# Kernel tuning notes

Hardware: AMD Instinct MI355X
Metric: run time of the kernel (lower is better)

## Reference

```python
import jax, jax.numpy as jnp
import numpy as np

N_NODES = 200000
N_EDGES = 800000
N_GRAPHS = 2048
N_SUB = 32768
E_SUB = 131072
F_IN = 38
H0, H1, H2 = 256, 128, 64
BN_EPS = 1e-5


def _l2norm(x):
    n = jnp.sqrt(jnp.sum(x * x, axis=1, keepdims=True))
    return x / jnp.maximum(n, 1e-12)


def _bn(x):
    # fresh nn.BatchNorm1d in training mode: gamma=1, beta=0, biased var
    m = x.mean(0, keepdims=True)
    v = x.var(0, keepdims=True)
    return (x - m) * jax.lax.rsqrt(v + BN_EPS)


def _seg_bn(x, seg, num_seg):
    # per-subgraph BatchNorm (source loops over subgraphs, BN stats per subgraph)
    ones = jnp.ones((x.shape[0],), x.dtype)
    cnt = jnp.maximum(jax.ops.segment_sum(ones, seg, num_seg), 1.0)[:, None]
    m = jax.ops.segment_sum(x, seg, num_seg) / cnt
    v = jax.ops.segment_sum(x * x, seg, num_seg) / cnt - m * m
    return (x - m[seg]) * jax.lax.rsqrt(jnp.maximum(v[seg], 0.0) + BN_EPS)


def _seg_mean(x, seg, num_seg):
    ones = jnp.ones((x.shape[0],), x.dtype)
    cnt = jnp.maximum(jax.ops.segment_sum(ones, seg, num_seg), 1.0)[:, None]
    return jax.ops.segment_sum(x, seg, num_seg) / cnt


def _gcn(x, W, b, src, dst):
    N = x.shape[0]
    h = x @ W
    deg = jnp.ones((N,), x.dtype).at[dst].add(1.0)  # in-degree + self loop
    dinv = jax.lax.rsqrt(deg)
    coef = (dinv[src] * dinv[dst])[:, None]
    agg = jnp.zeros_like(h).at[dst].add(coef * h[src]) + (dinv * dinv)[:, None] * h
    return agg + b


def setup_inputs() -> dict:
    key = jax.random.key(0)
    ks = jax.random.split(key, 40)

    def lin(k, fi, fo):
        return jax.random.normal(k, (fi, fo), jnp.float32) / np.float32(np.sqrt(fi))

    inp = {}
    inp['x'] = jax.random.normal(ks[0], (N_NODES, F_IN), jnp.float32)
    inp['edge_index'] = jax.random.randint(ks[1], (2, N_EDGES), 0, N_NODES)
    inp['batch'] = jnp.sort(jax.random.randint(ks[2], (N_NODES,), 0, N_GRAPHS))
    inp['target_x'] = jax.random.normal(ks[3], (N_GRAPHS, F_IN), jnp.float32)
    inp['pos_x'] = jax.random.normal(ks[4], (N_SUB, F_IN), jnp.float32)
    inp['pos_edge_index'] = jax.random.randint(ks[5], (2, E_SUB), 0, N_SUB)
    inp['pos_batch'] = jnp.sort(jax.random.randint(ks[6], (N_SUB,), 0, N_GRAPHS))
    inp['neg_x'] = jax.random.normal(ks[7], (N_SUB, F_IN), jnp.float32)
    inp['neg_edge_index'] = jax.random.randint(ks[8], (2, E_SUB), 0, N_SUB)
    inp['neg_batch'] = jnp.sort(jax.random.randint(ks[9], (N_SUB,), 0, N_GRAPHS))

    # main GCN encoder
    inp['enc_W0'] = lin(ks[10], F_IN, H0); inp['enc_b0'] = jnp.zeros((H0,), jnp.float32)
    inp['enc_W1'] = lin(ks[11], H0, H1);  inp['enc_b1'] = jnp.zeros((H1,), jnp.float32)
    inp['enc_W2'] = lin(ks[12], H1, H2);  inp['enc_b2'] = jnp.zeros((H2,), jnp.float32)
    # decoder (bias=False)
    inp['dec_W0'] = lin(ks[13], H2, H1)
    inp['dec_W1'] = lin(ks[14], H1, H0)
    inp['dec_W2'] = lin(ks[15], H0, F_IN)
    # node MLP encoder
    inp['node_W0'] = lin(ks[16], F_IN, H0); inp['node_b0'] = jnp.zeros((H0,), jnp.float32)
    inp['node_W1'] = lin(ks[17], H0, H1);  inp['node_b1'] = jnp.zeros((H1,), jnp.float32)
    inp['node_W2'] = lin(ks[18], H1, H2);  inp['node_b2'] = jnp.zeros((H2,), jnp.float32)
    # subgraph GCN encoder (last layer of encode_subgraph reuses self.encoders[-1])
    inp['sub_W0'] = lin(ks[19], F_IN, H0); inp['sub_b0'] = jnp.zeros((H0,), jnp.float32)
    inp['sub_W1'] = lin(ks[20], H0, H1);  inp['sub_b1'] = jnp.zeros((H1,), jnp.float32)
    # classifier
    inp['cls_W0'] = lin(ks[21], H2, H1);  inp['cls_b0'] = jnp.zeros((H1,), jnp.float32)
    inp['cls_W1'] = lin(ks[22], H1, 16);  inp['cls_b1'] = jnp.zeros((16,), jnp.float32)
    inp['cls_W2'] = lin(ks[23], 16, 1);   inp['cls_b2'] = jnp.zeros((1,), jnp.float32)
    return inp


def reference(x, edge_index, batch, target_x, pos_x, pos_edge_index, pos_batch,
              neg_x, neg_edge_index, neg_batch,
              enc_W0, enc_b0, enc_W1, enc_b1, enc_W2, enc_b2,
              dec_W0, dec_W1, dec_W2,
              node_W0, node_b0, node_W1, node_b1, node_W2, node_b2,
              sub_W0, sub_b0, sub_W1, sub_b1,
              cls_W0, cls_b0, cls_W1, cls_b1, cls_W2, cls_b2):
    relu = jax.nn.relu
    src, dst = edge_index[0], edge_index[1]

    # encode: GCN -> ReLU -> BN (x2), GCN, L2 normalize
    h = _bn(relu(_gcn(x, enc_W0, enc_b0, src, dst)))
    h = _bn(relu(_gcn(h, enc_W1, enc_b1, src, dst)))
    z = _l2norm(_gcn(h, enc_W2, enc_b2, src, dst))

    # decode: Linear(no bias) ReLU stack, sigmoid output
    r = relu(z @ dec_W0)
    r = relu(r @ dec_W1)
    x_recon = jax.nn.sigmoid(r @ dec_W2)

    z_pool = _seg_mean(z, batch, N_GRAPHS)

    # encode_node on target node features
    t = _bn(relu(target_x @ node_W0 + node_b0))
    t = _bn(relu(t @ node_W1 + node_b1))
    target_z = _l2norm(t @ node_W2 + node_b2)

    # batched subgraph encoding: GCN stack with per-subgraph BatchNorm;
    # last layer reuses main encoders[-1] weights (as in source encode_subgraph)
    def encode_sub(sx, sei, seg):
        s, d = sei[0], sei[1]
        sh = _seg_bn(relu(_gcn(sx, sub_W0, sub_b0, s, d)), seg, N_GRAPHS)
        sh = _seg_bn(relu(_gcn(sh, sub_W1, sub_b1, s, d)), seg, N_GRAPHS)
        return _l2norm(_gcn(sh, enc_W2, enc_b2, s, d))

    pos_z = encode_sub(pos_x, pos_edge_index, pos_batch)
    pos_pool = _seg_mean(pos_z, pos_batch, N_GRAPHS)
    neg_z = encode_sub(neg_x, neg_edge_index, neg_batch)
    neg_pool = _seg_mean(neg_z, neg_batch, N_GRAPHS)

    # classify negative subgraph pools
    p = relu(neg_pool @ cls_W0 + cls_b0)
    p = relu(p @ cls_W1 + cls_b1)
    neg_pred = jax.nn.sigmoid(p @ cls_W2 + cls_b2)

    return (x_recon, z_pool, target_z, pos_pool, neg_pool, neg_pred)
```

## Files before the change

### kernel.cpp

```cpp
#include <hip/hip_runtime.h>
#include <hip/hip_bf16.h>
#include <math.h>

#define N_NODES  200000
#define N_EDGES  800000
#define N_GRAPHS 2048
#define N_SUB    32768
#define E_SUB    131072
#define F_IN     38
#define H0       256
#define H1       128
#define H2       64
#define BN_EPS   1e-5f

typedef __hip_bfloat16 bf16;
typedef __attribute__((ext_vector_type(8))) short short8;
typedef __attribute__((ext_vector_type(4))) short short4v;
typedef __attribute__((ext_vector_type(4))) float float4v;

static __host__ __device__ inline int cdiv(int a, int b) { return (a + b - 1) / b; }

__device__ inline float ldf(const float* p, size_t i) { return p[i]; }
__device__ inline float ldf(const bf16* p, size_t i)  { return __bfloat162float(p[i]); }
__device__ inline void  stf(float* p, size_t i, float v) { p[i] = v; }
__device__ inline void  stf(bf16* p, size_t i, float v)  { p[i] = __float2bfloat16(v); }

__device__ inline float2 ldf2(const float* p, size_t i) { return ((const float2*)p)[i]; }
__device__ inline float2 ldf2(const bf16* p, size_t i) {
    __hip_bfloat162 v = ((const __hip_bfloat162*)p)[i];
    return make_float2(__bfloat162float(v.x), __bfloat162float(v.y));
}
__device__ inline void stf2(float* p, size_t i, float2 v) { ((float2*)p)[i] = v; }
__device__ inline void stf2(bf16* p, size_t i, float2 v) {
    __hip_bfloat162 t;
    t.x = __float2bfloat16(v.x);
    t.y = __float2bfloat16(v.y);
    ((__hip_bfloat162*)p)[i] = t;
}

__device__ inline short bf16bits(float v) {
    bf16 t = __float2bfloat16(v);
    return *reinterpret_cast<short*>(&t);
}
__device__ inline float bits2f(short s) {
    return __bfloat162float(*reinterpret_cast<const bf16*>(&s));
}

__global__ void k_zero(float* __restrict__ p, int n) {
    int i = blockIdx.x * 256 + threadIdx.x;
    if (i < n) p[i] = 0.f;
}

__global__ void k_count(const int* __restrict__ dst, int* __restrict__ cnt, int e) {
    int i = blockIdx.x * 256 + threadIdx.x;
    if (i < e) atomicAdd(&cnt[dst[i]], 1);
}

__global__ void k_dinv(const int* __restrict__ cnt, float* __restrict__ dinv, int n) {
    int i = blockIdx.x * 256 + threadIdx.x;
    if (i < n) dinv[i] = rsqrtf(1.0f + (float)cnt[i]);
}

__global__ void k_scan_sum(const int* __restrict__ cnt, int* __restrict__ bsum, int n) {
    __shared__ int tmp[256];
    int t = threadIdx.x;
    int i = blockIdx.x * 256 + t;
    tmp[t] = (i < n) ? cnt[i] : 0;
    __syncthreads();
    for (int off = 128; off > 0; off >>= 1) {
        if (t < off) tmp[t] += tmp[t + off];
        __syncthreads();
    }
    if (t == 0) bsum[blockIdx.x] = tmp[0];
}

__global__ void k_scan_top(int* __restrict__ bsum, int nb) {
    __shared__ int tmp[1024];
    int t = threadIdx.x;
    int v = (t < nb) ? bsum[t] : 0;
    tmp[t] = v;
    __syncthreads();
    for (int off = 1; off < 1024; off <<= 1) {
        int a = (t >= off) ? tmp[t - off] : 0;
        __syncthreads();
        tmp[t] += a;
        __syncthreads();
    }
    if (t < nb) bsum[t] = tmp[t] - v;
}

__global__ void k_scan_apply(const int* __restrict__ cnt, const int* __restrict__ bsum,
                             int* __restrict__ rowptr, int n) {
    __shared__ int tmp[256];
    int t = threadIdx.x;
    int i = blockIdx.x * 256 + t;
    int v = (i < n) ? cnt[i] : 0;
    tmp[t] = v;
    __syncthreads();
    for (int off = 1; off < 256; off <<= 1) {
        int a = (t >= off) ? tmp[t - off] : 0;
        __syncthreads();
        tmp[t] += a;
        __syncthreads();
    }
    int excl = tmp[t] - v + bsum[blockIdx.x];
    if (i < n) rowptr[i] = excl;
    if (i == n - 1) rowptr[n] = excl + v;
}

__global__ void k_fill(const int* __restrict__ src, const int* __restrict__ dst,
                       const int* __restrict__ rowptr, int* __restrict__ cursor,
                       int* __restrict__ col, int e) {
    int i = blockIdx.x * 256 + threadIdx.x;
    if (i < e) {
        int d = dst[i];
        int p = rowptr[d] + atomicAdd(&cursor[d], 1);
        col[p] = src[i];
    }
}

__global__ void k_gbound(const int* __restrict__ seg, int n, int nseg,
                         int* __restrict__ gstart) {
    int i = blockIdx.x * 256 + threadIdx.x;
    if (i >= n) return;
    int s = seg[i];
    if (i == 0) {
        for (int g = 0; g <= s; ++g) gstart[g] = 0;
    } else {
        int p = seg[i - 1];
        for (int g = p + 1; g <= s; ++g) gstart[g] = i;
    }
    if (i == n - 1) {
        for (int g = s + 1; g <= nseg; ++g) gstart[g] = n;
    }
}

__global__ void k_merge(const float* __restrict__ px, const float* __restrict__ nx,
                        const int* __restrict__ pei, const int* __restrict__ nei,
                        const int* __restrict__ pb, const int* __restrict__ nbt,
                        float* __restrict__ mx, int* __restrict__ msrc,
                        int* __restrict__ mdst, int* __restrict__ mb) {
    int stride = gridDim.x * 256;
    for (int i = blockIdx.x * 256 + threadIdx.x; i < N_SUB * F_IN; i += stride) {
        mx[i] = px[i];
        mx[(size_t)N_SUB * F_IN + i] = nx[i];
    }
    for (int i = blockIdx.x * 256 + threadIdx.x; i < E_SUB; i += stride) {
        msrc[i] = pei[i];
        mdst[i] = pei[E_SUB + i];
        msrc[E_SUB + i] = nei[i] + N_SUB;
        mdst[E_SUB + i] = nei[E_SUB + i] + N_SUB;
    }
    for (int i = blockIdx.x * 256 + threadIdx.x; i < N_SUB; i += stride) {
        mb[i] = pb[i];
        mb[N_SUB + i] = nbt[i] + N_GRAPHS;
    }
}

template <typename TI, typename TO, int PPN>
__global__ __launch_bounds__(256) void k_gather5(
    const TI* __restrict__ h, const float* __restrict__ dinv,
    const int* __restrict__ rowptr, const int* __restrict__ col,
    TO* __restrict__ o, int n, int M2, int S2,
    const float* __restrict__ bias, int relu)
{
    const int NPW = 64 / PPN;
    int g0 = threadIdx.x / PPN;
    int pr = threadIdx.x % PPN;
    int nA = (blockIdx.x * 4 + threadIdx.y) * (2 * NPW) + g0 * 2;
    if (nA >= n) return;
    int nB = nA + 1;
    bool okB = nB < n;
    bool pld = pr < M2, pst = pr < S2;

    int2 rp = *(const int2*)(rowptr + nA);
    float diA = dinv[nA];
    float diB = okB ? dinv[nB] : 0.f;
    float2 vsA = make_float2(0.f, 0.f), vsB = make_float2(0.f, 0.f);
    if (pld) {
        vsA = ldf2(h, (size_t)nA * M2 + pr);
        if (okB) vsB = ldf2(h, (size_t)nB * M2 + pr);
    }
    int peB = okB ? rowptr[nA + 2] : rp.y;

    int pA = rp.x, peA = rp.y;
    int pB = peA;

    int sA1 = 0, sB1 = 0;
    float dA0 = 0.f, dB0 = 0.f;
    float2 vA0 = make_float2(0.f, 0.f), vB0 = make_float2(0.f, 0.f);

    if (pA < peA) {
        int s0 = col[pA];
        sA1 = (pA + 1 < peA) ? col[pA + 1] : 0;
        dA0 = dinv[s0];
        if (pld) vA0 = ldf2(h, (size_t)s0 * M2 + pr);
    }
    if (pB < peB) {
        int s0 = col[pB];
        sB1 = (pB + 1 < peB) ? col[pB + 1] : 0;
        dB0 = dinv[s0];
        if (pld) vB0 = ldf2(h, (size_t)s0 * M2 + pr);
    }

    float2 accA, accB;
    accA.x = diA * diA * vsA.x; accA.y = diA * diA * vsA.y;
    accB.x = diB * diB * vsB.x; accB.y = diB * diB * vsB.y;

    while (pA < peA && pB < peB) {
        int sA2 = (pA + 2 < peA) ? col[pA + 2] : 0;
        int sB2 = (pB + 2 < peB) ? col[pB + 2] : 0;
        float2 vA1 = (pA + 1 < peA && pld) ? ldf2(h, (size_t)sA1 * M2 + pr)
                                           : make_float2(0.f, 0.f);
        float2 vB1 = (pB + 1 < peB && pld) ? ldf2(h, (size_t)sB1 * M2 + pr)
                                           : make_float2(0.f, 0.f);
        float dA1 = (pA + 1 < peA) ? dinv[sA1] : 0.f;
        float dB1 = (pB + 1 < peB) ? dinv[sB1] : 0.f;
        float cfA = dA0 * diA, cfB = dB0 * diB;
        accA.x += cfA * vA0.x; accA.y += cfA * vA0.y;
        accB.x += cfB * vB0.x; accB.y += cfB * vB0.y;
        sA1 = sA2; vA0 = vA1; dA0 = dA1;
        sB1 = sB2; vB0 = vB1; dB0 = dB1;
        ++pA; ++pB;
    }
    while (pA < peA) {
        int sA2 = (pA + 2 < peA) ? col[pA + 2] : 0;
        float2 vA1 = (pA + 1 < peA && pld) ? ldf2(h, (size_t)sA1 * M2 + pr)
                                           : make_float2(0.f, 0.f);
        float dA1 = (pA + 1 < peA) ? dinv[sA1] : 0.f;
        float cfA = dA0 * diA;
        accA.x += cfA * vA0.x; accA.y += cfA * vA0.y;
        sA1 = sA2; vA0 = vA1; dA0 = dA1; ++pA;
    }
    while (pB < peB) {
        int sB2 = (pB + 2 < peB) ? col[pB + 2] : 0;
        float2 vB1 = (pB + 1 < peB && pld) ? ldf2(h, (size_t)sB1 * M2 + pr)
                                           : make_float2(0.f, 0.f);
        float dB1 = (pB + 1 < peB) ? dinv[sB1] : 0.f;
        float cfB = dB0 * diB;
        accB.x += cfB * vB0.x; accB.y += cfB * vB0.y;
        sB1 = sB2; vB0 = vB1; dB0 = dB1; ++pB;
    }

    if (pst) {
        float2 rA = accA;
        if (bias && pld) { rA.x += bias[2 * pr]; rA.y += bias[2 * pr + 1]; }
        if (relu) { rA.x = fmaxf(rA.x, 0.f); rA.y = fmaxf(rA.y, 0.f); }
        stf2(o, (size_t)nA * S2 + pr, rA);
        if (okB) {
            float2 rB = accB;
            if (bias && pld) { rB.x += bias[2 * pr]; rB.y += bias[2 * pr + 1]; }
            if (relu) { rB.x = fmaxf(rB.x, 0.f); rB.y = fmaxf(rB.y, 0.f); }
            stf2(o, (size_t)nB * S2 + pr, rB);
        }
    }
}

template <typename TI, typename TO>
static void launch_gather(const TI* h, const float* dinv, const int* rowptr,
                          const int* col, TO* o, int n, int M, int Sout,
                          const float* bias, int relu, hipStream_t stream) {
    dim3 b(64, 4);
    int M2 = M >> 1, S2 = Sout >> 1;
    if (S2 > 32)
        k_gather5<TI, TO, 64><<<cdiv(n, 8), b, 0, stream>>>(h, dinv, rowptr, col, o,
                                                            n, M2, S2, bias, relu);
    else
        k_gather5<TI, TO, 32><<<cdiv(n, 16), b, 0, stream>>>(h, dinv, rowptr, col, o,
                                                             n, M2, S2, bias, relu);
}

template <typename TO, int LPR>
__global__ __launch_bounds__(256) void k_gather6(
    const bf16* __restrict__ h, const float* __restrict__ dinv,
    const int* __restrict__ rowptr, const int* __restrict__ col,
    TO* __restrict__ o, int n, const float* __restrict__ bias, int relu)
{
    const int W = LPR * 8;
    const int NG = 64 / LPR;
    const int g = threadIdx.x / LPR;
    const int c0 = (threadIdx.x % LPR) * 8;
    const int nA = (blockIdx.x * 4 + threadIdx.y) * (2 * NG) + g * 2;
    const int nB = nA + 1;
    if (nA >= n) return;
    const bool okB = nB < n;

    int2 rp = *(const int2*)(rowptr + nA);
    int peB = okB ? rowptr[nB + 1] : rp.y;
    float diA = dinv[nA];
    float diB = okB ? dinv[nB] : 0.f;
    short8 zed = {0, 0, 0, 0, 0, 0, 0, 0};
    short8 slA = *(const short8*)(h + (size_t)nA * W + c0);
    short8 slB = okB ? *(const short8*)(h + (size_t)nB * W + c0) : zed;

    int pA = rp.x, peA = rp.y;
    int pB = rp.y;

    float accA[8], accB[8];
    float qA = diA * diA, qB = diB * diB;
#pragma unroll
    for (int j = 0; j < 8; ++j) {
        accA[j] = qA * bits2f(slA[j]);
        accB[j] = qB * bits2f(slB[j]);
    }

    int sA1 = 0, sB1 = 0;
    float dA0 = 0.f, dB0 = 0.f;
    short8 vA0 = zed, vB0 = zed;
    if (pA < peA) {
        int s0 = col[pA];
        sA1 = (pA + 1 < peA) ? col[pA + 1] : 0;
        dA0 = dinv[s0];
        vA0 = *(const short8*)(h + (size_t)s0 * W + c0);
    }
    if (pB < peB) {
        int s0 = col[pB];
        sB1 = (pB + 1 < peB) ? col[pB + 1] : 0;
        dB0 = dinv[s0];
        vB0 = *(const short8*)(h + (size_t)s0 * W + c0);
    }

    while (__any(pA < peA || pB < peB)) {
        if (pA < peA) {
            int sA2 = (pA + 2 < peA) ? col[pA + 2] : 0;
            short8 vA1 = zed;
            float dA1 = 0.f;
            if (pA + 1 < peA) {
                vA1 = *(const short8*)(h + (size_t)sA1 * W + c0);
                dA1 = dinv[sA1];
            }
            float cf = dA0 * diA;
#pragma unroll
            for (int j = 0; j < 8; ++j) accA[j] += cf * bits2f(vA0[j]);
            vA0 = vA1; dA0 = dA1; sA1 = sA2; ++pA;
        }
        if (pB < peB) {
            int sB2 = (pB + 2 < peB) ? col[pB + 2] : 0;
            short8 vB1 = zed;
            float dB1 = 0.f;
            if (pB + 1 < peB) {
                vB1 = *(const short8*)(h + (size_t)sB1 * W + c0);
                dB1 = dinv[sB1];
            }
            float cf = dB0 * diB;
#pragma unroll
            for (int j = 0; j < 8; ++j) accB[j] += cf * bits2f(vB0[j]);
            vB0 = vB1; dB0 = dB1; sB1 = sB2; ++pB;
        }
    }

    float bv[8];
#pragma unroll
    for (int j = 0; j < 8; ++j) bv[j] = 0.f;
    if (bias) {
        float4 b0 = *(const float4*)(bias + c0);
        float4 b1 = *(const float4*)(bias + c0 + 4);
        bv[0] = b0.x; bv[1] = b0.y; bv[2] = b0.z; bv[3] = b0.w;
        bv[4] = b1.x; bv[5] = b1.y; bv[6] = b1.z; bv[7] = b1.w;
    }

    auto store_row = [&](int node, float* acc) {
        float r[8];
#pragma unroll
        for (int j = 0; j < 8; ++j) {
            r[j] = acc[j] + bv[j];
            if (relu) r[j] = fmaxf(r[j], 0.f);
        }
        size_t off = (size_t)node * W + c0;
        if constexpr (sizeof(TO) == 2) {
            short8 pk;
#pragma unroll
            for (int j = 0; j < 8; ++j) pk[j] = bf16bits(r[j]);
            *(short8*)((bf16*)o + off) = pk;
        } else {
            float4 f0 = {r[0], r[1], r[2], r[3]};
            float4 f1 = {r[4], r[5], r[6], r[7]};
            *(float4*)((float*)o + off) = f0;
            *(float4*)((float*)o + off + 4) = f1;
        }
    };
    store_row(nA, accA);
    if (okB) store_row(nB, accB);
}

template <typename TO>
static void launch_gather6(const bf16* h, const float* dinv, const int* rowptr,
                           const int* col, TO* o, int n, int W,
                           const float* bias, int relu, hipStream_t stream) {
    dim3 b(64, 4);
    if (W == 128)
        k_gather6<TO, 16><<<cdiv(n, 32), b, 0, stream>>>(h, dinv, rowptr, col, o, n,
                                                         bias, relu);
    else
        k_gather6<TO, 8><<<cdiv(n, 64), b, 0, stream>>>(h, dinv, rowptr, col, o, n,
                                                        bias, relu);
}

template <int K, int M, int Mp>
__device__ inline void wpack1(const float* __restrict__ W, bf16* __restrict__ o, int j) {
    int kk = j & 31;
    int rem = j >> 5;
    int ncol = rem % Mp;
    int s = rem / Mp;
    int k = s * 32 + kk;
    float v = (k < K && ncol < M) ? W[(size_t)k * M + ncol] : 0.f;
    o[j] = __float2bfloat16(v);
}

__global__ void k_wpack_all(const float* __restrict__ eW0, const float* __restrict__ eW1,
                            const float* __restrict__ eW2, const float* __restrict__ dW0,
                            const float* __restrict__ dW1, const float* __restrict__ dW2,
                            const float* __restrict__ sW0, const float* __restrict__ sW1,
                            bf16* __restrict__ arena) {
    for (int i = blockIdx.x * 256 + threadIdx.x; i < 159744; i += gridDim.x * 256) {
        if (i < 16384)       wpack1<38, 256, 256>(eW0, arena, i);
        else if (i < 49152)  wpack1<256, 128, 128>(eW1, arena + 16384, i - 16384);
        else if (i < 57344)  wpack1<128, 64, 64>(eW2, arena + 49152, i - 49152);
        else if (i < 65536)  wpack1<64, 128, 128>(dW0, arena + 57344, i - 57344);
        else if (i < 98304)  wpack1<128, 256, 256>(dW1, arena + 65536, i - 65536);
        else if (i < 110592) wpack1<256, 38, 48>(dW2, arena + 98304, i - 98304);
        else if (i < 126976) wpack1<38, 256, 256>(sW0, arena + 110592, i - 110592);
        else                 wpack1<256, 128, 128>(sW1, arena + 126976, i - 126976);
    }
}

template <int K, int M, int Mp>
__global__ void k_wfold(const float* __restrict__ W, const float* __restrict__ mu,
                        const float* __restrict__ sc, bf16* __restrict__ Wb,
                        float* __restrict__ bout) {
    const int tot = (K / 32) * Mp * 32;
    for (int i = blockIdx.x * 256 + threadIdx.x; i < tot; i += gridDim.x * 256) {
        int kk = i & 31;
        int rem = i >> 5;
        int ncol = rem % Mp;
        int s = rem / Mp;
        int k = s * 32 + kk;
        float v = (k < K && ncol < M) ? sc[k] * W[(size_t)k * M + ncol] : 0.f;
        Wb[i] = __float2bfloat16(v);
    }
    if (blockIdx.x == 0 && threadIdx.x < M) {
        int j = threadIdx.x;
        float s = 0.f;
        for (int k = 0; k < K; ++k) s -= mu[k] * sc[k] * W[(size_t)k * M + j];
        bout[j] = s;
    }
}

template <typename TC, int NT, int S, int BNM>
__global__ __launch_bounds__(256, 3) void k_mfma_gemm(
    const bf16* __restrict__ A, const bf16* __restrict__ Wb,
    TC* __restrict__ C, int M, int MC,
    const float* __restrict__ bias, int act,
    const float* __restrict__ mu, const float* __restrict__ sc,
    const int* __restrict__ seg)
{
    const int SA = S * 32;
    const int Mp = NT * 16;
    const int lane = threadIdx.x;
    const int wave = threadIdx.y;
    const int row0 = blockIdx.x * 64 + wave * 16;
    const int qr = lane >> 4;
    const int lc = lane & 15;

    short8 af[S];
    {
        const bf16* arow = A + (size_t)(row0 + lc) * SA + qr * 8;
#pragma unroll
        for (int s = 0; s < S; ++s) af[s] = *(const short8*)(arow + s * 32);
    }
    if (BNM == 2) {
        size_t bnbase = (size_t)seg[row0 + lc] * SA;
#pragma unroll
        for (int s = 0; s < S; ++s) {
            int kb = s * 32 + qr * 8;
            const float* mp = mu + bnbase + kb;
            const float* sp = sc + bnbase + kb;
            float4 m0 = *(const float4*)mp, m1 = *(const float4*)(mp + 4);
            float4 s0 = *(const float4*)sp, s1 = *(const float4*)(sp + 4);
            float av[8];
#pragma unroll
            for (int j = 0; j < 8; ++j) av[j] = bits2f(af[s][j]);
            av[0] = (av[0] - m0.x) * s0.x; av[1] = (av[1] - m0.y) * s0.y;
            av[2] = (av[2] - m0.z) * s0.z; av[3] = (av[3] - m0.w) * s0.w;
            av[4] = (av[4] - m1.x) * s1.x; av[5] = (av[5] - m1.y) * s1.y;
            av[6] = (av[6] - m1.z) * s1.z; av[7] = (av[7] - m1.w) * s1.w;
#pragma unroll
            for (int j = 0; j < 8; ++j) af[s][j] = bf16bits(av[j]);
        }
    }

    float4v acc[NT];
#pragma unroll
    for (int t = 0; t < NT; ++t) acc[t] = (float4v){0.f, 0.f, 0.f, 0.f};

    const bf16* wrow = Wb + (size_t)lc * 32 + qr * 8;
#pragma unroll
    for (int s = 0; s < S; ++s) {
        short8 wfv[NT];
#pragma unroll
        for (int t = 0; t < NT; ++t)
            wfv[t] = *(const short8*)(wrow + ((size_t)s * Mp + t * 16) * 32);
#pragma unroll
        for (int t = 0; t < NT; ++t)
            acc[t] = __builtin_amdgcn_mfma_f32_16x16x32_bf16(wfv[t], af[s], acc[t], 0, 0, 0);
    }

    const int row = row0 + lc;
#pragma unroll
    for (int t = 0; t < NT; ++t) {
        int c0 = t * 16 + qr * 4;
        if (c0 >= M) continue;
        float v[4];
#pragma unroll
        for (int r = 0; r < 4; ++r) v[r] = acc[t][r];
        if (bias) {
            if (c0 + 3 < M) {
                float4 bv = *(const float4*)(bias + c0);
                v[0] += bv.x; v[1] += bv.y; v[2] += bv.z; v[3] += bv.w;
            } else {
#pragma unroll
                for (int r = 0; r < 4; ++r) if (c0 + r < M) v[r] += bias[c0 + r];
            }
        }
#pragma unroll
        for (int r = 0; r < 4; ++r) {
            if (act == 1) v[r] = fmaxf(v[r], 0.f);
            else if (act == 2) v[r] = 1.f / (1.f + expf(-v[r]));
        }
        if (c0 + 3 < M) {
            if constexpr (sizeof(TC) == 2) {
                short4v pk = {bf16bits(v[0]), bf16bits(v[1]), bf16bits(v[2]), bf16bits(v[3])};
                *(short4v*)((bf16*)C + (size_t)row * MC + c0) = pk;
            } else {
                stf2((float*)C, ((size_t)row * MC + c0) >> 1, make_float2(v[0], v[1]));
                stf2((float*)C, ((size_t)row * MC + c0 + 2) >> 1, make_float2(v[2], v[3]));
            }
        } else {
#pragma unroll
            for (int r = 0; r < 4; ++r)
                if (c0 + r < M) stf(C, (size_t)row * MC + c0 + r, v[r]);
        }
    }
}

template <typename TC, int BNM>
static void launch_mfma(const bf16* A, const bf16* Wb, TC* C, int n, int SA,
                        int Mp, int M, int MC, const float* bias, int act,
                        const float* mu, const float* sc, const int* seg,
                        hipStream_t stream) {
    dim3 b(64, 4);
    int g = n / 64;
    if (SA == 64 && Mp == 256)
        k_mfma_gemm<TC, 16, 2, BNM><<<g, b, 0, stream>>>(A, Wb, C, M, MC, bias, act, mu, sc, seg);
    else if (SA == 256 && Mp == 128)
        k_mfma_gemm<TC, 8, 8, BNM><<<g, b, 0, stream>>>(A, Wb, C, M, MC, bias, act, mu, sc, seg);
    else if (SA == 128 && Mp == 64)
        k_mfma_gemm<TC, 4, 4, BNM><<<g, b, 0, stream>>>(A, Wb, C, M, MC, bias, act, mu, sc, seg);
}

__global__ __launch_bounds__(256) void k_l0stats(
    const bf16* __restrict__ Y0, const bf16* __restrict__ W0b,
    const float* __restrict__ b0, float* __restrict__ sum,
    float* __restrict__ sumsq, int ntiles)
{
    __shared__ float ls[4][512];
    const int lane = threadIdx.x;
    const int wave = threadIdx.y;
    const int lc = lane & 15, qr = lane >> 4;

    float bv[16];
#pragma unroll
    for (int t = 0; t < 16; ++t) bv[t] = b0[t * 16 + lc];

    float sReg[16], qReg[16];
#pragma unroll
    for (int t = 0; t < 16; ++t) { sReg[t] = 0.f; qReg[t] = 0.f; }

    for (int tile = blockIdx.x; tile < ntiles; tile += gridDim.x) {
        const int row0 = tile * 64 + wave * 16;
        const bf16* arow = Y0 + (size_t)(row0 + lc) * 64 + qr * 8;
        float4v acc[16];
#pragma unroll
        for (int t = 0; t < 16; ++t) acc[t] = (float4v){0.f, 0.f, 0.f, 0.f};
#pragma unroll
        for (int s = 0; s < 2; ++s) {
            short8 af = *(const short8*)(arow + s * 32);
#pragma unroll
            for (int t = 0; t < 16; ++t) {
                short8 wf = *(const short8*)(W0b + ((size_t)(s * 256 + t * 16 + lc)) * 32 + qr * 8);
                acc[t] = __builtin_amdgcn_mfma_f32_16x16x32_bf16(af, wf, acc[t], 0, 0, 0);
            }
        }
#pragma unroll
        for (int t = 0; t < 16; ++t) {
            float s4 = 0.f, q4 = 0.f;
#pragma unroll
            for (int r = 0; r < 4; ++r) {
                float v = fmaxf(acc[t][r] + bv[t], 0.f);
                v = bits2f(bf16bits(v));
                s4 += v;
                q4 += v * v;
            }
            s4 += __shfl_xor(s4, 16, 64); s4 += __shfl_xor(s4, 32, 64);
            q4 += __shfl_xor(q4, 16, 64); q4 += __shfl_xor(q4, 32, 64);
            sReg[t] += s4;
            qReg[t] += q4;
        }
    }
    if (lane < 16) {
#pragma unroll
        for (int t = 0; t < 16; ++t) {
            ls[wave][t * 16 + lc] = sReg[t];
            ls[wave][256 + t * 16 + lc] = qReg[t];
        }
    }
    __syncthreads();
    int tid = wave * 64 + lane;
    if (tid < 256) {
        atomicAdd(&sum[tid], ls[0][tid] + ls[1][tid] + ls[2][tid] + ls[3][tid]);
        atomicAdd(&sumsq[tid],
                  ls[0][256 + tid] + ls[1][256 + tid] + ls[2][256 + tid] + ls[3][256 + tid]);
    }
}

__global__ __launch_bounds__(256, 3) void k_fused01(
    const bf16* __restrict__ Y0, const bf16* __restrict__ W0b,
    const float* __restrict__ b0, const bf16* __restrict__ W1b,
    const float* __restrict__ b1f, bf16* __restrict__ G1, int n)
{
    __shared__ __attribute__((aligned(16))) char lds[4][8192];
    const int lane = threadIdx.x;
    const int wave = threadIdx.y;
    const int lc = lane & 15, qr = lane >> 4;
    const int row0 = blockIdx.x * 64 + wave * 16;
    char* r2 = lds[wave];
    const int swz = (lc & 7) << 4;

    {
        const bf16* arow = Y0 + (size_t)(row0 + lc) * 64 + qr * 8;
        short8 af0 = *(const short8*)(arow);
        short8 af1 = *(const short8*)(arow + 32);
        float4v acc[16];
#pragma unroll
        for (int t = 0; t < 16; ++t) acc[t] = (float4v){0.f, 0.f, 0.f, 0.f};
#pragma unroll
        for (int s = 0; s < 2; ++s) {
            short8 af = s ? af1 : af0;
            short8 wfv[16];
#pragma unroll
            for (int t = 0; t < 16; ++t)
                wfv[t] = *(const short8*)(W0b + ((size_t)(s * 256 + t * 16 + lc)) * 32 + qr * 8);
#pragma unroll
            for (int t = 0; t < 16; ++t)
                acc[t] = __builtin_amdgcn_mfma_f32_16x16x32_bf16(wfv[t], af, acc[t], 0, 0, 0);
        }
#pragma unroll
        for (int t = 0; t < 16; ++t) {
            int c0 = t * 16 + qr * 4;
            float4 bv = *(const float4*)(b0 + c0);
            short4v pk = {bf16bits(fmaxf(acc[t][0] + bv.x, 0.f)),
                          bf16bits(fmaxf(acc[t][1] + bv.y, 0.f)),
                          bf16bits(fmaxf(acc[t][2] + bv.z, 0.f)),
                          bf16bits(fmaxf(acc[t][3] + bv.w, 0.f))};
            int off = lc * 512 + t * 32 + qr * 8;
            *(short4v*)(r2 + (off ^ swz)) = pk;
        }
    }

    short8 afv[8];
#pragma unroll
    for (int s = 0; s < 8; ++s) {
        int off = lc * 512 + s * 64 + qr * 16;
        afv[s] = *(const short8*)(r2 + (off ^ swz));
    }
    float4v a2[8];
#pragma unroll
    for (int t = 0; t < 8; ++t) a2[t] = (float4v){0.f, 0.f, 0.f, 0.f};
#pragma unroll
    for (int s = 0; s < 8; ++s) {
        short8 wfv[8];
#pragma unroll
        for (int t = 0; t < 8; ++t)
            wfv[t] = *(const short8*)(W1b + ((size_t)(s * 128 + t * 16 + lc)) * 32 + qr * 8);
#pragma unroll
        for (int t = 0; t < 8; ++t)
            a2[t] = __builtin_amdgcn_mfma_f32_16x16x32_bf16(wfv[t], afv[s], a2[t], 0, 0, 0);
    }
    const int row = row0 + lc;
#pragma unroll
    for (int t = 0; t < 8; ++t) {
        int c0 = t * 16 + qr * 4;
        float4 bv = *(const float4*)(b1f + c0);
        short4v pk = {bf16bits(a2[t][0] + bv.x), bf16bits(a2[t][1] + bv.y),
                      bf16bits(a2[t][2] + bv.z), bf16bits(a2[t][3] + bv.w)};
        *(short4v*)(G1 + (size_t)row * 128 + c0) = pk;
    }
}

__global__ __launch_bounds__(256, 3) void k_decoder(
    const bf16* __restrict__ zb, const bf16* __restrict__ dW0b,
    const bf16* __restrict__ dW1b, const bf16* __restrict__ dW2b,
    float* __restrict__ xrec, int n)
{
    __shared__ __attribute__((aligned(16))) char lds[4][12288];
    const int lane = threadIdx.x;
    const int wave = threadIdx.y;
    const int lc = lane & 15, qr = lane >> 4;
    const int row0 = blockIdx.x * 64 + wave * 16;
    char* r1 = lds[wave];
    char* r2 = lds[wave] + 4096;
    const int swz = (lc & 7) << 4;

    {
        const bf16* arow = zb + (size_t)(row0 + lc) * 64 + qr * 8;
        short8 af0 = *(const short8*)(arow);
        short8 af1 = *(const short8*)(arow + 32);
        float4v a1[8];
#pragma unroll
        for (int t = 0; t < 8; ++t) a1[t] = (float4v){0.f, 0.f, 0.f, 0.f};
#pragma unroll
        for (int s = 0; s < 2; ++s) {
            short8 af = s ? af1 : af0;
            short8 wfv[8];
#pragma unroll
            for (int t = 0; t < 8; ++t)
                wfv[t] = *(const short8*)(dW0b + ((size_t)(s * 128 + t * 16 + lc)) * 32 + qr * 8);
#pragma unroll
            for (int t = 0; t < 8; ++t)
                a1[t] = __builtin_amdgcn_mfma_f32_16x16x32_bf16(wfv[t], af, a1[t], 0, 0, 0);
            __builtin_amdgcn_sched_group_barrier(0x020, 8, 0);
            __builtin_amdgcn_sched_group_barrier(0x008, 8, 0);
        }
#pragma unroll
        for (int t = 0; t < 8; ++t) {
            short4v pk = {bf16bits(fmaxf(a1[t][0], 0.f)), bf16bits(fmaxf(a1[t][1], 0.f)),
                          bf16bits(fmaxf(a1[t][2], 0.f)), bf16bits(fmaxf(a1[t][3], 0.f))};
            int off = lc * 256 + t * 32 + qr * 8;
            *(short4v*)(r1 + (off ^ swz)) = pk;
        }
    }

    {
        short8 afv[4];
#pragma unroll
        for (int s = 0; s < 4; ++s) {
            int off = lc * 256 + s * 64 + qr * 16;
            afv[s] = *(const short8*)(r1 + (off ^ swz));
        }
        float4v a2[16];
#pragma unroll
        for (int t = 0; t < 16; ++t) a2[t] = (float4v){0.f, 0.f, 0.f, 0.f};
#pragma unroll
        for (int s = 0; s < 4; ++s) {
#pragma unroll
            for (int h = 0; h < 2; ++h) {
                short8 wfv[8];
#pragma unroll
                for (int tt = 0; tt < 8; ++tt) {
                    int t = h * 8 + tt;
                    wfv[tt] = *(const short8*)(dW1b + ((size_t)(s * 256 + t * 16 + lc)) * 32 + qr * 8);
                }
#pragma unroll
                for (int tt = 0; tt < 8; ++tt) {
                    int t = h * 8 + tt;
                    a2[t] = __builtin_amdgcn_mfma_f32_16x16x32_bf16(wfv[tt], afv[s], a2[t], 0, 0, 0);
                }
                __builtin_amdgcn_sched_group_barrier(0x020, 8, 0);
                __builtin_amdgcn_sched_group_barrier(0x008, 8, 0);
            }
        }
#pragma unroll
        for (int t = 0; t < 16; ++t) {
            short4v pk = {bf16bits(fmaxf(a2[t][0], 0.f)), bf16bits(fmaxf(a2[t][1], 0.f)),
                          bf16bits(fmaxf(a2[t][2], 0.f)), bf16bits(fmaxf(a2[t][3], 0.f))};
            int off = lc * 512 + t * 32 + qr * 8;
            *(short4v*)(r2 + (off ^ swz)) = pk;
        }
    }

    short8 afv[8];
#pragma unroll
    for (int s = 0; s < 8; ++s) {
        int off = lc * 512 + s * 64 + qr * 16;
        afv[s] = *(const short8*)(r2 + (off ^ swz));
    }
    float4v a3[3];
#pragma unroll
    for (int t = 0; t < 3; ++t) a3[t] = (float4v){0.f, 0.f, 0.f, 0.f};
#pragma unroll
    for (int s = 0; s < 8; ++s) {
        short8 wfv[3];
#pragma unroll
        for (int t = 0; t < 3; ++t)
            wfv[t] = *(const short8*)(dW2b + ((size_t)(s * 48 + t * 16 + lc)) * 32 + qr * 8);
#pragma unroll
        for (int t = 0; t < 3; ++t)
            a3[t] = __builtin_amdgcn_mfma_f32_16x16x32_bf16(wfv[t], afv[s], a3[t], 0, 0, 0);
        __builtin_amdgcn_sched_group_barrier(0x020, 3, 0);
        __builtin_amdgcn_sched_group_barrier(0x008, 3, 0);
    }
    float* orow = xrec + (size_t)(row0 + lc) * 38;
#pragma unroll
    for (int t = 0; t < 3; ++t) {
        int c0 = t * 16 + qr * 4;
        float v0 = 1.f / (1.f + expf(-a3[t][0]));
        float v1 = 1.f / (1.f + expf(-a3[t][1]));
        float v2 = 1.f / (1.f + expf(-a3[t][2]));
        float v3 = 1.f / (1.f + expf(-a3[t][3]));
        if (c0 + 1 < 38) *(float2*)(orow + c0) = make_float2(v0, v1);
        if (c0 + 3 < 38) *(float2*)(orow + c0 + 2) = make_float2(v2, v3);
    }
}

template <typename TA, typename TC, int NJ>
__global__ __launch_bounds__(256) void k_gemm(
    const TA* __restrict__ A, const float* __restrict__ W,
    TC* __restrict__ C, int n, int K, int M,
    const float* __restrict__ bias, int act,
    const float* __restrict__ mu, const float* __restrict__ sc)
{
    __shared__ float alds[64 * 32];
    __shared__ float wlds[32 * 256];
    const int l = threadIdx.x;
    const int wy = threadIdx.y;
    const int tid = wy * 64 + l;
    const int row0 = blockIdx.x * 64;

    float acc[16][NJ];
#pragma unroll
    for (int r = 0; r < 16; ++r)
#pragma unroll
        for (int j = 0; j < NJ; ++j) acc[r][j] = 0.f;

    int cidx[NJ]; bool jval[NJ];
#pragma unroll
    for (int j = 0; j < NJ; ++j) {
        cidx[j] = l + 64 * j;
        jval[j] = cidx[j] < M;
    }

    for (int k0 = 0; k0 < K; k0 += 32) {
        int kt = min(32, K - k0);
        __syncthreads();
        for (int i = tid; i < 64 * 32; i += 256) {
            int r = i >> 5, kk = i & 31;
            int row = row0 + r, k = k0 + kk;
            float v = (row < n && k < K) ? ldf(A, (size_t)row * K + k) : 0.f;
            if (mu && k < K) v = (v - mu[k]) * sc[k];
            alds[i] = v;
        }
        for (int i = tid; i < kt * M; i += 256)
            wlds[i] = W[(size_t)k0 * M + i];
        if (kt < 32)
            for (int i = kt * M + tid; i < 32 * M; i += 256) wlds[i] = 0.f;
        __syncthreads();

#pragma unroll 2
        for (int kkg = 0; kkg < 8; ++kkg) {
            float wv[4][NJ];
#pragma unroll
            for (int q = 0; q < 4; ++q)
#pragma unroll
                for (int j = 0; j < NJ; ++j)
                    wv[q][j] = jval[j] ? wlds[(kkg * 4 + q) * M + cidx[j]] : 0.f;
#pragma unroll
            for (int rr = 0; rr < 16; ++rr) {
                const float4* arow = (const float4*)&alds[(wy * 16 + rr) * 32];
                float4 av = arow[kkg];
#pragma unroll
                for (int j = 0; j < NJ; ++j) {
                    acc[rr][j] += av.x * wv[0][j];
                    acc[rr][j] += av.y * wv[1][j];
                    acc[rr][j] += av.z * wv[2][j];
                    acc[rr][j] += av.w * wv[3][j];
                }
            }
        }
    }

#pragma unroll
    for (int rr = 0; rr < 16; ++rr) {
        int row = row0 + wy * 16 + rr;
        if (row >= n) continue;
#pragma unroll
        for (int j = 0; j < NJ; ++j) {
            if (!jval[j]) continue;
            float v = acc[rr][j];
            if (bias) v += bias[cidx[j]];
            if (act == 1) v = fmaxf(v, 0.f);
            else if (act == 2) v = 1.f / (1.f + expf(-v));
            stf(C, (size_t)row * M + cidx[j], v);
        }
    }
}

template <typename T>
__global__ __launch_bounds__(256) void k_bn_stats8(
    const T* __restrict__ x, int n, int M,
    float* __restrict__ sum, float* __restrict__ sumsq)
{
    __shared__ float ls[512];
    int t = threadIdx.x;
    for (int i = t; i < 2 * M; i += 256) ls[i] = 0.f;
    __syncthreads();

    int gpr = M >> 3;
    int c8 = (t % gpr) * 8;
    int g = t / gpr;
    int rpb = 256 / gpr;

    float s[8], q[8];
#pragma unroll
    for (int j = 0; j < 8; ++j) { s[j] = 0.f; q[j] = 0.f; }

    for (int r = blockIdx.x * rpb + g; r < n; r += gridDim.x * rpb) {
        float v[8];
        if constexpr (sizeof(T) == 2) {
            short8 v8 = *(const short8*)((const bf16*)x + (size_t)r * M + c8);
#pragma unroll
            for (int j = 0; j < 8; ++j) v[j] = bits2f(v8[j]);
        } else {
            float4 f0 = *(const float4*)((const float*)x + (size_t)r * M + c8);
            float4 f1 = *(const float4*)((const float*)x + (size_t)r * M + c8 + 4);
            v[0] = f0.x; v[1] = f0.y; v[2] = f0.z; v[3] = f0.w;
            v[4] = f1.x; v[5] = f1.y; v[6] = f1.z; v[7] = f1.w;
        }
#pragma unroll
        for (int j = 0; j < 8; ++j) { s[j] += v[j]; q[j] += v[j] * v[j]; }
    }
#pragma unroll
    for (int j = 0; j < 8; ++j) {
        atomicAdd(&ls[c8 + j], s[j]);
        atomicAdd(&ls[M + c8 + j], q[j]);
    }
    __syncthreads();
    for (int i = t; i < M; i += 256) {
        atomicAdd(&sum[i], ls[i]);
        atomicAdd(&sumsq[i], ls[M + i]);
    }
}

__global__ void k_bn_fin(float* __restrict__ sum, float* __restrict__ sumsq, int n, int M) {
    int c = threadIdx.x;
    if (c < M) {
        float m = sum[c] / (float)n;
        float v = fmaxf(sumsq[c] / (float)n - m * m, 0.f);
        sum[c] = m;
        sumsq[c] = rsqrtf(v + BN_EPS);
    }
}

template <int CPL>
__global__ __launch_bounds__(256) void k_segbn(
    const bf16* __restrict__ x, const int* __restrict__ gstart, int nseg,
    float* __restrict__ mu, float* __restrict__ sc)
{
    const int M = 64 * CPL;
    int s = blockIdx.x * 4 + threadIdx.y;
    if (s >= nseg) return;
    int l = threadIdx.x;
    int gs = gstart[s], ge = gstart[s + 1];
    float sum[CPL], sq[CPL];
#pragma unroll
    for (int j = 0; j < CPL; ++j) { sum[j] = 0.f; sq[j] = 0.f; }
    for (int r = gs; r < ge; ++r) {
        const bf16* px = x + (size_t)r * M + l * CPL;
        if constexpr (CPL == 4) {
            short4v v4 = *(const short4v*)px;
#pragma unroll
            for (int j = 0; j < 4; ++j) {
                float v = bits2f(v4[j]);
                sum[j] += v; sq[j] += v * v;
            }
        } else {
            __hip_bfloat162 v2 = *(const __hip_bfloat162*)px;
            float v0 = __bfloat162float(v2.x), v1 = __bfloat162float(v2.y);
            sum[0] += v0; sq[0] += v0 * v0;
            sum[1] += v1; sq[1] += v1 * v1;
        }
    }
    float c = fmaxf((float)(ge - gs), 1.f);
#pragma unroll
    for (int j = 0; j < CPL; ++j) {
        float m = sum[j] / c;
        float v = fmaxf(sq[j] / c - m * m, 0.f);
        mu[(size_t)s * M + l * CPL + j] = m;
        sc[(size_t)s * M + l * CPL + j] = rsqrtf(v + BN_EPS);
    }
}

__global__ __launch_bounds__(256) void k_pool(
    const float* __restrict__ z, const int* __restrict__ gstart, int nseg,
    float* __restrict__ o)
{
    int s = blockIdx.x * 4 + threadIdx.y;
    if (s >= nseg) return;
    int l = threadIdx.x;
    int gs = gstart[s], ge = gstart[s + 1];
    float acc = 0.f;
    for (int r = gs; r < ge; ++r) acc += z[(size_t)r * 64 + l];
    o[(size_t)s * 64 + l] = acc / fmaxf((float)(ge - gs), 1.f);
}

__global__ __launch_bounds__(256) void k_l2pool(
    const float* __restrict__ zs, const int* __restrict__ gstart, int nseg,
    float* __restrict__ o)
{
    int s = blockIdx.x * 4 + threadIdx.y;
    if (s >= nseg) return;
    int l = threadIdx.x;
    int gs = gstart[s], ge = gstart[s + 1];
    float acc = 0.f;
    for (int r = gs; r < ge; ++r) {
        float v = zs[(size_t)r * 64 + l];
        float ss = v * v;
        for (int off = 32; off > 0; off >>= 1) ss += __shfl_xor(ss, off, 64);
        acc += v / fmaxf(sqrtf(ss), 1e-12f);
    }
    o[(size_t)s * 64 + l] = acc / fmaxf((float)(ge - gs), 1.f);
}

__global__ void k_l2norm2(float* __restrict__ x, bf16* __restrict__ xb, int n) {
    int row = blockIdx.x * 4 + threadIdx.y;
    if (row >= n) return;
    int l = threadIdx.x;
    float v = x[(size_t)row * 64 + l];
    float ss = v * v;
    for (int o = 32; o > 0; o >>= 1) ss += __shfl_xor(ss, o, 64);
    float r = v / fmaxf(sqrtf(ss), 1e-12f);
    x[(size_t)row * 64 + l] = r;
    if (xb) xb[(size_t)row * 64 + l] = __float2bfloat16(r);
}

template <typename TA, typename TC>
static void launch_gemm(const TA* A, const float* W, TC* C, int n, int K, int M,
                        const float* bias, int act, const float* mu, const float* sc,
                        hipStream_t stream) {
    dim3 b(64, 4);
    int g = cdiv(n, 64);
    int nj = (M + 63) >> 6;
    if (nj >= 4)      k_gemm<TA, TC, 4><<<g, b, 0, stream>>>(A, W, C, n, K, M, bias, act, mu, sc);
    else if (nj == 2) k_gemm<TA, TC, 2><<<g, b, 0, stream>>>(A, W, C, n, K, M, bias, act, mu, sc);
    else              k_gemm<TA, TC, 1><<<g, b, 0, stream>>>(A, W, C, n, K, M, bias, act, mu, sc);
}

extern "C" void kernel_launch(void* const* d_in, const int* in_sizes, int n_in,
                              void* d_out, int out_size, void* d_ws, size_t ws_size,
                              hipStream_t stream) {
    const float* x        = (const float*)d_in[0];
    const int*   ei       = (const int*)  d_in[1];
    const int*   batch    = (const int*)  d_in[2];
    const float* target_x = (const float*)d_in[3];
    const float* pos_x    = (const float*)d_in[4];
    const int*   pos_ei   = (const int*)  d_in[5];
    const int*   pos_b    = (const int*)  d_in[6];
    const float* neg_x    = (const float*)d_in[7];
    const int*   neg_ei   = (const int*)  d_in[8];
    const int*   neg_b    = (const int*)  d_in[9];
    const float* enc_W0 = (const float*)d_in[10]; const float* enc_b0 = (const float*)d_in[11];
    const float* enc_W1 = (const float*)d_in[12]; const float* enc_b1 = (const float*)d_in[13];
    const float* enc_W2 = (const float*)d_in[14]; const float* enc_b2 = (const float*)d_in[15];
    const float* dec_W0 = (const float*)d_in[16];
    const float* dec_W1 = (const float*)d_in[17];
    const float* dec_W2 = (const float*)d_in[18];
    const float* node_W0 = (const float*)d_in[19]; const float* node_b0 = (const float*)d_in[20];
    const float* node_W1 = (const float*)d_in[21]; const float* node_b1 = (const float*)d_in[22];
    const float* node_W2 = (const float*)d_in[23]; const float* node_b2 = (const float*)d_in[24];
    const float* sub_W0 = (const float*)d_in[25]; const float* sub_b0 = (const float*)d_in[26];
    const float* sub_W1 = (const float*)d_in[27]; const float* sub_b1 = (const float*)d_in[28];
    const float* cls_W0 = (const float*)d_in[29]; const float* cls_b0 = (const float*)d_in[30];
    const float* cls_W1 = (const float*)d_in[31]; const float* cls_b1 = (const float*)d_in[32];
    const float* cls_W2 = (const float*)d_in[33]; const float* cls_b2 = (const float*)d_in[34];

    float* out = (float*)d_out;
    const size_t OFF_XREC  = 0;
    const size_t OFF_ZPOOL = (size_t)N_NODES * F_IN;
    const size_t OFF_TZ    = OFF_ZPOOL + (size_t)N_GRAPHS * H2;
    const size_t OFF_PPOOL = OFF_TZ    + (size_t)N_GRAPHS * H2;
    const size_t OFF_NPOOL = OFF_PPOOL + (size_t)N_GRAPHS * H2;
    const size_t OFF_PRED  = OFF_NPOOL + (size_t)N_GRAPHS * H2;

    char* wsp = (char*)d_ws;
    auto alloc = [&](size_t nfloats) -> float* {
        float* p = (float*)wsp;
        wsp += ((nfloats + 63) / 64) * 64 * sizeof(float);
        return p;
    };
    float* R1     = alloc((size_t)N_NODES * 128);
    float* R2     = alloc((size_t)N_NODES * 128);
    float* dinv   = alloc(N_NODES);
    int*   cnt    = (int*)alloc(N_NODES);
    int*   rowptr = (int*)alloc(N_NODES + 1);
    int*   bsum   = (int*)alloc(1024);
    int*   ccol   = (int*)alloc(N_EDGES);
    float* ssum   = alloc(256);
    float* ssumsq = alloc(256);
    bf16*  wpk    = (bf16*)alloc(101 * 1024);
    float* bfold  = alloc(256);
    (void)ws_size; (void)in_sizes; (void)n_in; (void)out_size;

    bf16* eW0b = wpk;
    bf16* eW1b = eW0b + 16384;
    bf16* eW2b = eW1b + 32768;
    bf16* dW0b = eW2b + 8192;
    bf16* dW1b = dW0b + 8192;
    bf16* dW2b = dW1b + 32768;
    bf16* sW0b = dW2b + 12288;
    bf16* sW1b = sW0b + 16384;
    bf16* fW1b = sW1b + 32768;
    bf16* fW2b = fW1b + 32768;

    float* tailf    = R2 + (size_t)16 * 1024 * 1024;
    float* segsumM  = tailf;
    float* segsumqM = tailf + (size_t)1048576;
    float* mx       = tailf + (size_t)2097152;
    int*   msrc     = (int*)(mx + (size_t)2 * N_SUB * F_IN);
    int*   mdst     = msrc + 2 * E_SUB;
    int*   mb       = mdst + 2 * E_SUB;
    int*   gstartM  = mb + 2 * N_SUB;
    int*   gstart2k = gstartM + 4112;

    dim3 b64x4(64, 4);
    auto zero = [&](void* p, size_t nfloats) {
        k_zero<<<cdiv((int)nfloats, 256), 256, 0, stream>>>((float*)p, (int)nfloats);
    };

    k_wpack_all<<<624, 256, 0, stream>>>(enc_W0, enc_W1, enc_W2, dec_W0, dec_W1,
                                         dec_W2, sub_W0, sub_W1, wpk);

    auto build_graph = [&](const int* srcp, const int* dstp, int n, int e) {
        zero(cnt, n);
        k_count<<<cdiv(e, 256), 256, 0, stream>>>(dstp, cnt, e);
        k_dinv<<<cdiv(n, 256), 256, 0, stream>>>(cnt, dinv, n);
        int nb = cdiv(n, 256);
        k_scan_sum<<<nb, 256, 0, stream>>>(cnt, bsum, n);
        k_scan_top<<<1, 1024, 0, stream>>>(bsum, nb);
        k_scan_apply<<<nb, 256, 0, stream>>>(cnt, bsum, rowptr, n);
        zero(cnt, n);
        k_fill<<<cdiv(e, 256), 256, 0, stream>>>(srcp, dstp, rowptr, cnt, ccol, e);
    };

    auto bn_stats = [&](auto* xx, int n, int M) {
        zero(ssum, 512);
        int rpb = 256 / (M >> 3);
        int g = min(512, cdiv(n, rpb));
        k_bn_stats8<<<g, 256, 0, stream>>>(xx, n, M, ssum, ssumsq);
        k_bn_fin<<<1, 256, 0, stream>>>(ssum, ssumsq, n, M);
    };

    build_graph(ei, ei + N_EDGES, N_NODES, N_EDGES);

    bf16* Y0 = (bf16*)R1;
    launch_gather<float, bf16>(x, dinv, rowptr, ccol, Y0, N_NODES, F_IN, 64,
                               nullptr, 0, stream);

    zero(ssum, 512);
    k_l0stats<<<512, b64x4, 0, stream>>>(Y0, eW0b, enc_b0, ssum, ssumsq,
                                         N_NODES / 64);
    k_bn_fin<<<1, 256, 0, stream>>>(ssum, ssumsq, N_NODES, H0);
    k_wfold<256, 128, 128><<<128, 256, 0, stream>>>(enc_W1, ssum, ssumsq, fW1b, bfold);

    bf16* G1 = (bf16*)R2;
    k_fused01<<<N_NODES / 64, b64x4, 0, stream>>>(Y0, eW0b, enc_b0, fW1b, bfold,
                                                  G1, N_NODES);

    bf16* a1 = (bf16*)R1;
    launch_gather6<bf16>(G1, dinv, rowptr, ccol, a1, N_NODES, 128, enc_b1, 1, stream);
    bn_stats(a1, N_NODES, H1);
    k_wfold<128, 64, 64><<<32, 256, 0, stream>>>(enc_W2, ssum, ssumsq, fW2b, bfold + 128);

    bf16* G2 = (bf16*)R2;
    launch_mfma<bf16, 0>(a1, fW2b, G2, N_NODES, 128, 64, H2, H2, bfold + 128, 0,
                         nullptr, nullptr, nullptr, stream);
    float* z  = R1;
    bf16*  zb = (bf16*)(R1 + (size_t)N_NODES * 64);
    launch_gather6<float>(G2, dinv, rowptr, ccol, z, N_NODES, 64, enc_b2, 0, stream);
    k_l2norm2<<<cdiv(N_NODES, 4), b64x4, 0, stream>>>(z, zb, N_NODES);

    k_gbound<<<cdiv(N_NODES, 256), 256, 0, stream>>>(batch, N_NODES, N_GRAPHS, gstart2k);
    k_pool<<<cdiv(N_GRAPHS, 4), b64x4, 0, stream>>>(z, gstart2k, N_GRAPHS,
                                                    out + OFF_ZPOOL);

    k_decoder<<<N_NODES / 64, b64x4, 0, stream>>>(zb, dW0b, dW1b, dW2b,
                                                  out + OFF_XREC, N_NODES);

    float* t0 = R2;
    launch_gemm<float, float>(target_x, node_W0, t0, N_GRAPHS, F_IN, H0, node_b0, 1,
                              nullptr, nullptr, stream);
    bn_stats(t0, N_GRAPHS, H0);
    float* t1 = R1;
    launch_gemm<float, float>(t0, node_W1, t1, N_GRAPHS, H0, H1, node_b1, 1,
                              ssum, ssumsq, stream);
    bn_stats(t1, N_GRAPHS, H1);
    launch_gemm<float, float>(t1, node_W2, out + OFF_TZ, N_GRAPHS, H1, H2, node_b2, 0,
                              ssum, ssumsq, stream);
    k_l2norm2<<<cdiv(N_GRAPHS, 4), b64x4, 0, stream>>>(out + OFF_TZ, nullptr, N_GRAPHS);

    k_merge<<<2048, 256, 0, stream>>>(pos_x, neg_x, pos_ei, neg_ei, pos_b, neg_b,
                                      mx, msrc, mdst, mb);
    const int NS2 = 2 * N_SUB, ES2 = 2 * E_SUB, NG2 = 2 * N_GRAPHS;
    build_graph(msrc, mdst, NS2, ES2);
    k_gbound<<<cdiv(NS2, 256), 256, 0, stream>>>(mb, NS2, NG2, gstartM);

    bf16* Ys = (bf16*)R2;
    launch_gather<float, bf16>(mx, dinv, rowptr, ccol, Ys, NS2, F_IN, 64,
                               nullptr, 0, stream);
    bf16* as0 = (bf16*)R1;
    launch_mfma<bf16, 0>(Ys, sW0b, as0, NS2, 64, 256, H0, H0, sub_b0, 1,
                         nullptr, nullptr, nullptr, stream);
    k_segbn<4><<<cdiv(NG2, 4), b64x4, 0, stream>>>(as0, gstartM, NG2,
                                                   segsumM, segsumqM);

    bf16* Gs1 = (bf16*)R2;
    launch_mfma<bf16, 2>(as0, sW1b, Gs1, NS2, 256, 128, H1, H1, nullptr, 0,
                         segsumM, segsumqM, mb, stream);
    bf16* as1 = (bf16*)R1;
    launch_gather6<bf16>(Gs1, dinv, rowptr, ccol, as1, NS2, 128, sub_b1, 1, stream);
    k_segbn<2><<<cdiv(NG2, 4), b64x4, 0, stream>>>(as1, gstartM, NG2,
                                                   segsumM, segsumqM);

    bf16* Gs2 = (bf16*)R2;
    launch_mfma<bf16, 2>(as1, eW2b, Gs2, NS2, 128, 64, H2, H2, nullptr, 0,
                         segsumM, segsumqM, mb, stream);
    float* zs = R1;
    launch_gather6<float>(Gs2, dinv, rowptr, ccol, zs, NS2, 64, enc_b2, 0, stream);
    k_l2pool<<<cdiv(NG2, 4), b64x4, 0, stream>>>(zs, gstartM, NG2, out + OFF_PPOOL);

    float* c1 = R2;
    launch_gemm<float, float>(out + OFF_NPOOL, cls_W0, c1, N_GRAPHS, H2, H1, cls_b0, 1,
                              nullptr, nullptr, stream);
    float* c2 = R1;
    launch_gemm<float, float>(c1, cls_W1, c2, N_GRAPHS, H1, 16, cls_b1, 1,
                              nullptr, nullptr, stream);
    launch_gemm<float, float>(c2, cls_W2, out + OFF_PRED, N_GRAPHS, 16, 1, cls_b2, 2,
                              nullptr, nullptr, stream);
}
```

Measured before the change: 1.178 ms.

## Stage MFMA weight tiles in padded LDS shared across waves

The generic MFMA GEMM and the fused layer-0/1 kernel now copy weight fragments cooperatively into a padded LDS buffer (80-byte row stride) in blocks. Each wave then reads its B operands from LDS instead of issuing per-wave global loads. This is meant to cut redundant global and L2 traffic for weights that all four waves share. In exchange it adds block-wide barriers, uses more LDS, and lowers the fused kernel's launch-bounds occupancy hint from 3 to 2.

Measured after the change: 1.128 ms. -4.2%, faster.

```diff
diff --git a/kernel.cpp b/kernel.cpp
--- a/kernel.cpp
+++ b/kernel.cpp
@@ -44,6 +44,17 @@
 }
 __device__ inline float bits2f(short s) {
     return __bfloat162float(*reinterpret_cast<const bf16*>(&s));
+}
+
+__device__ inline void stage_w(const bf16* __restrict__ src, char* dst,
+                               int nchunk, int tid) {
+    for (int c = tid; c < nchunk; c += 256) {
+        short8 v = *(const short8*)(src + c * 8);
+        *(short8*)(dst + ((c >> 2) * 80 + (c & 3) * 16)) = v;
+    }
+}
+__device__ inline short8 wstage_read(const char* w, int r, int qr) {
+    return *(const short8*)(w + r * 80 + qr * 16);
 }
 
 __global__ void k_zero(float* __restrict__ p, int n) {
@@ -456,8 +467,13 @@
 {
     const int SA = S * 32;
     const int Mp = NT * 16;
+    const int SBLK = (16384 / (Mp * 32) < S) ? (16384 / (Mp * 32)) : S;
+    const int RPS = SBLK * Mp;
+    __shared__ __attribute__((aligned(16))) char wstage[RPS * 80];
+
     const int lane = threadIdx.x;
     const int wave = threadIdx.y;
+    const int tid = wave * 64 + lane;
     const int row0 = blockIdx.x * 64 + wave * 16;
     const int qr = lane >> 4;
     const int lc = lane & 15;
@@ -493,16 +509,20 @@
 #pragma unroll
     for (int t = 0; t < NT; ++t) acc[t] = (float4v){0.f, 0.f, 0.f, 0.f};
 
-    const bf16* wrow = Wb + (size_t)lc * 32 + qr * 8;
-#pragma unroll
-    for (int s = 0; s < S; ++s) {
-        short8 wfv[NT];
-#pragma unroll
-        for (int t = 0; t < NT; ++t)
-            wfv[t] = *(const short8*)(wrow + ((size_t)s * Mp + t * 16) * 32);
-#pragma unroll
-        for (int t = 0; t < NT; ++t)
-            acc[t] = __builtin_amdgcn_mfma_f32_16x16x32_bf16(wfv[t], af[s], acc[t], 0, 0, 0);
+#pragma unroll
+    for (int s0 = 0; s0 < S; s0 += SBLK) {
+        if (s0) __syncthreads();
+        stage_w(Wb + (size_t)s0 * Mp * 32, wstage, RPS * 4, tid);
+        __syncthreads();
+#pragma unroll
+        for (int sl = 0; sl < SBLK; ++sl) {
+#pragma unroll
+            for (int t = 0; t < NT; ++t) {
+                short8 wf = wstage_read(wstage, sl * Mp + t * 16 + lc, qr);
+                acc[t] = __builtin_amdgcn_mfma_f32_16x16x32_bf16(wf, af[s0 + sl],
+                                                                 acc[t], 0, 0, 0);
+            }
+        }
     }
 
     const int row = row0 + lc;
@@ -623,36 +643,39 @@
     }
 }
 
-__global__ __launch_bounds__(256, 3) void k_fused01(
+__global__ __launch_bounds__(256, 2) void k_fused01(
     const bf16* __restrict__ Y0, const bf16* __restrict__ W0b,
     const float* __restrict__ b0, const bf16* __restrict__ W1b,
     const float* __restrict__ b1f, bf16* __restrict__ G1, int n)
 {
-    __shared__ __attribute__((aligned(16))) char lds[4][8192];
+    __shared__ __attribute__((aligned(16))) char wstage[40960];
+    __shared__ __attribute__((aligned(16))) char a0buf[4][8192];
     const int lane = threadIdx.x;
     const int wave = threadIdx.y;
+    const int tid = wave * 64 + lane;
     const int lc = lane & 15, qr = lane >> 4;
     const int row0 = blockIdx.x * 64 + wave * 16;
-    char* r2 = lds[wave];
+    char* r2 = a0buf[wave];
     const int swz = (lc & 7) << 4;
 
+    stage_w(W0b, wstage, 2048, tid);
+    const bf16* arow = Y0 + (size_t)(row0 + lc) * 64 + qr * 8;
+    short8 af0 = *(const short8*)(arow);
+    short8 af1 = *(const short8*)(arow + 32);
+    __syncthreads();
+
     {
-        const bf16* arow = Y0 + (size_t)(row0 + lc) * 64 + qr * 8;
-        short8 af0 = *(const short8*)(arow);
-        short8 af1 = *(const short8*)(arow + 32);
         float4v acc[16];
 #pragma unroll
         for (int t = 0; t < 16; ++t) acc[t] = (float4v){0.f, 0.f, 0.f, 0.f};
 #pragma unroll
         for (int s = 0; s < 2; ++s) {
             short8 af = s ? af1 : af0;
-            short8 wfv[16];
-#pragma unroll
-            for (int t = 0; t < 16; ++t)
-                wfv[t] = *(const short8*)(W0b + ((size_t)(s * 256 + t * 16 + lc)) * 32 + qr * 8);
-#pragma unroll
-            for (int t = 0; t < 16; ++t)
-                acc[t] = __builtin_amdgcn_mfma_f32_16x16x32_bf16(wfv[t], af, acc[t], 0, 0, 0);
+#pragma unroll
+            for (int t = 0; t < 16; ++t) {
+                short8 wf = wstage_read(wstage, s * 256 + t * 16 + lc, qr);
+                acc[t] = __builtin_amdgcn_mfma_f32_16x16x32_bf16(wf, af, acc[t], 0, 0, 0);
+            }
         }
 #pragma unroll
         for (int t = 0; t < 16; ++t) {
@@ -677,14 +700,19 @@
 #pragma unroll
     for (int t = 0; t < 8; ++t) a2[t] = (float4v){0.f, 0.f, 0.f, 0.f};
 #pragma unroll
-    for (int s = 0; s < 8; ++s) {
-        short8 wfv[8];
-#pragma unroll
-        for (int t = 0; t < 8; ++t)
-            wfv[t] = *(const short8*)(W1b + ((size_t)(s * 128 + t * 16 + lc)) * 32 + qr * 8);
-#pragma unroll
-        for (int t = 0; t < 8; ++t)
-            a2[t] = __builtin_amdgcn_mfma_f32_16x16x32_bf16(wfv[t], afv[s], a2[t], 0, 0, 0);
+    for (int h = 0; h < 2; ++h) {
+        __syncthreads();
+        stage_w(W1b + h * 16384, wstage, 2048, tid);
+        __syncthreads();
+#pragma unroll
+        for (int sl = 0; sl < 4; ++sl) {
+            int s = h * 4 + sl;
+#pragma unroll
+            for (int t = 0; t < 8; ++t) {
+                short8 wf = wstage_read(wstage, sl * 128 + t * 16 + lc, qr);
+                a2[t] = __builtin_amdgcn_mfma_f32_16x16x32_bf16(wf, afv[s], a2[t], 0, 0, 0);
+            }
+        }
     }
     const int row = row0 + lc;
 #pragma unroll
```
